# Kernel optimization log

Hardware: AMD Instinct MI355X
Metric: run time of the kernel (lower is better)

The kernel has to match this reference:

```python
import jax, jax.numpy as jnp
import numpy as np

B = 256      # events
N_SV = 64    # secondary vertices per event
N_TRK = 512  # tracks per event
N_PFC = 512  # PF candidates per event
K = 8        # kNN neighbors
H = 32       # hidden dim


def _lin_init(key, fan_in, fan_out):
    k1, k2 = jax.random.split(key)
    lim = 1.0 / np.sqrt(fan_in)
    W = jax.random.uniform(k1, (fan_in, fan_out), minval=-lim, maxval=lim, dtype=jnp.float32)
    b = jax.random.uniform(k2, (fan_out,), minval=-lim, maxval=lim, dtype=jnp.float32)
    return W, b


def setup_inputs() -> dict:
    key = jax.random.key(0)
    ks = jax.random.split(key, 16)
    inp = {
        'x_sv': jax.random.normal(ks[0], (B * N_SV, 14), dtype=jnp.float32),
        'x_trk': jax.random.normal(ks[1], (B * N_TRK, 30), dtype=jnp.float32),
        'x_pfc': jax.random.normal(ks[2], (B * N_PFC, 10), dtype=jnp.float32),
        'batch_sv': jnp.repeat(jnp.arange(B, dtype=jnp.int64), N_SV),
        'batch_trk': jnp.repeat(jnp.arange(B, dtype=jnp.int64), N_TRK),
        'batch_pfc': jnp.repeat(jnp.arange(B, dtype=jnp.int64), N_PFC),
    }
    inp['sv_W1'], inp['sv_b1'] = _lin_init(ks[3], 14, H)
    inp['sv_W2'], inp['sv_b2'] = _lin_init(ks[4], H, H)
    inp['trk_W1'], inp['trk_b1'] = _lin_init(ks[5], 30, H)
    inp['trk_W2'], inp['trk_b2'] = _lin_init(ks[6], H, H)
    inp['pfc_W1'], inp['pfc_b1'] = _lin_init(ks[7], 10, H)
    inp['pfc_W2'], inp['pfc_b2'] = _lin_init(ks[8], H, H)
    inp['conv_W'], inp['conv_b'] = _lin_init(ks[9], 2 * H, H)  # the single shared self.conv
    inp['out_W1'], inp['out_b1'] = _lin_init(ks[10], H, H)
    inp['out_W2'], inp['out_b2'] = _lin_init(ks[11], H, 1)
    return inp


def _encode(x, W1, b1, W2, b2):
    h = jax.nn.elu(x @ W1 + b1)
    return jax.nn.elu(h @ W2 + b2)


def _edge_conv(x_src, x_dst, W, b):
    # x_src [B,Ns,H] source set, x_dst [B,Nd,H] destination/query set.
    # kNN: for each dst node, K nearest src nodes (per event) by Euclidean dist.
    d2 = (jnp.sum(x_dst * x_dst, -1)[:, :, None]
          - 2.0 * jnp.einsum('bnd,bmd->bnm', x_dst, x_src)
          + jnp.sum(x_src * x_src, -1)[:, None, :])  # [B,Nd,Ns]
    _, idx = jax.lax.top_k(-d2, K)                     # [B,Nd,K]
    x_j = jax.vmap(lambda s, i: s[i])(x_src, idx)      # [B,Nd,K,H]
    x_i = jnp.broadcast_to(x_dst[:, :, None, :], x_j.shape)
    e = jnp.concatenate([x_i, x_j - x_i], axis=-1)     # [B,Nd,K,2H]
    m = jax.nn.elu(e @ W + b)                          # edge MLP
    return jnp.max(m, axis=2)                          # max aggregation [B,Nd,H]


def reference(x_sv, x_trk, x_pfc, batch_sv, batch_trk, batch_pfc,
              sv_W1, sv_b1, sv_W2, sv_b2,
              trk_W1, trk_b1, trk_W2, trk_b2,
              pfc_W1, pfc_b1, pfc_W2, pfc_b2,
              conv_W, conv_b, out_W1, out_b1, out_W2, out_b2):
    sv = _encode(x_sv, sv_W1, sv_b1, sv_W2, sv_b2).reshape(B, N_SV, H)
    trk = _encode(x_trk, trk_W1, trk_b1, trk_W2, trk_b2).reshape(B, N_TRK, H)
    pfc = _encode(x_pfc, pfc_W1, pfc_b1, pfc_W2, pfc_b2).reshape(B, N_PFC, H)

    feats1 = _edge_conv(sv, trk, conv_W, conv_b)     # sv -> trk
    feats2 = _edge_conv(pfc, trk, conv_W, conv_b)    # pfc -> trk
    feats3 = _edge_conv(feats1, feats2, conv_W, conv_b)  # feats1 -> feats2 (both trk-sized)

    # avg_pool_x(batch_trk, feats3, batch_trk): per-event mean
    f = feats3.reshape(B * N_TRK, H)
    s = jax.ops.segment_sum(f, batch_trk, num_segments=B)
    cnt = jax.ops.segment_sum(jnp.ones((B * N_TRK,), f.dtype), batch_trk, num_segments=B)
    pooled = s / cnt[:, None]

    out = jax.nn.sigmoid(jax.nn.elu(pooled @ out_W1 + out_b1) @ out_W2 + out_b2)  # [B,1]
    return out, jnp.arange(B, dtype=jnp.int64)
```

## Files before the change

kernel.cpp:

```cpp
#include <hip/hip_runtime.h>
#include <math.h>

#define NB 256
#define KNN 8

typedef __attribute__((ext_vector_type(8))) short short8;
typedef __attribute__((ext_vector_type(4))) float f32x4;

__device__ __forceinline__ float elu_f(float x) {
    return x > 0.f ? x : __expf(x) - 1.f;
}

__device__ __forceinline__ unsigned bf16rn(float x) {
    unsigned u = __float_as_uint(x);
    return (u + 0x7FFFu + ((u >> 16) & 1u)) >> 16;
}

__device__ __forceinline__ void bfsplit(float x, short& h, short& l) {
    unsigned hu = bf16rn(x);
    h = (short)hu;
    l = (short)bf16rn(x - __uint_as_float(hu << 16));
}

__device__ __forceinline__ void cex(unsigned& a, unsigned& b) {
    unsigned lo = min(a, b), hi = max(a, b);
    a = lo; b = hi;
}

__device__ __forceinline__ void sort4(unsigned* s) {
    cex(s[0], s[1]); cex(s[2], s[3]);
    cex(s[0], s[2]); cex(s[1], s[3]);
    cex(s[1], s[2]);
}

__device__ __forceinline__ void merge8_4(unsigned* v, const unsigned* s) {
    v[4] = min(v[4], s[3]); v[5] = min(v[5], s[2]);
    v[6] = min(v[6], s[1]); v[7] = min(v[7], s[0]);
    cex(v[0], v[4]); cex(v[1], v[5]); cex(v[2], v[6]); cex(v[3], v[7]);
    cex(v[0], v[2]); cex(v[1], v[3]); cex(v[4], v[6]); cex(v[5], v[7]);
    cex(v[0], v[1]); cex(v[2], v[3]); cex(v[4], v[5]); cex(v[6], v[7]);
}

__device__ __forceinline__ void merge8(unsigned* v, const unsigned* s) {
#pragma unroll
    for (int i = 0; i < 8; i++) v[i] = min(v[i], s[7 - i]);
    cex(v[0], v[4]); cex(v[1], v[5]); cex(v[2], v[6]); cex(v[3], v[7]);
    cex(v[0], v[2]); cex(v[1], v[3]); cex(v[4], v[6]); cex(v[5], v[7]);
    cex(v[0], v[1]); cex(v[2], v[3]); cex(v[4], v[5]); cex(v[6], v[7]);
}

template<int FIN, int MODE>
__device__ void encode_mfma_body(const float* __restrict__ x,
    const float* __restrict__ W1, const float* __restrict__ b1,
    const float* __restrict__ W2, const float* __restrict__ b2,
    const float* __restrict__ conv_W, const float* __restrict__ conv_b,
    float* __restrict__ enc, float* __restrict__ e1, float* __restrict__ e2,
    unsigned short* __restrict__ hiP, unsigned short* __restrict__ loP,
    float* __restrict__ nrmP,
    int blk, float* __restrict__ sx)
{
    int tid = threadIdx.x;
    int lane = tid & 63, wv = tid >> 6;
    int c = lane & 15, kg = lane >> 4;
    size_t node0 = (size_t)blk * 256;

    {
        const float* xb = x + node0 * FIN;
        for (int i = tid; i < 8192; i += 256) {
            int n = i >> 5, f = i & 31;
            sx[i] = (f < FIN) ? xb[n * FIN + f] : 0.f;
        }
    }
    __syncthreads();

    int rb = wv * 64;

#pragma unroll
    for (int ph = 0; ph < 3; ph++) {
        short8 Bh0, Bl0, Bh1, Bl1;
#pragma unroll
        for (int e = 0; e < 8; e++) {
            int kk = kg * 8 + e;
            float w0, w1;
            if (ph == 0) {
                w0 = (kk < FIN) ? W1[kk * 32 + c] : 0.f;
                w1 = (kk < FIN) ? W1[kk * 32 + 16 + c] : 0.f;
            } else if (ph == 1) {
                w0 = W2[kk * 32 + c];
                w1 = W2[kk * 32 + 16 + c];
            } else {
                w0 = conv_W[1024 + kk * 32 + c];
                w1 = conv_W[1024 + kk * 32 + 16 + c];
                if (MODE == 1) {
                    w0 = conv_W[kk * 32 + c] - w0;
                    w1 = conv_W[kk * 32 + 16 + c] - w1;
                }
            }
            short h, l;
            bfsplit(w0, h, l); Bh0[e] = h; Bl0[e] = l;
            bfsplit(w1, h, l); Bh1[e] = h; Bl1[e] = l;
        }
        float bias0, bias1;
        if (ph == 0)      { bias0 = b1[c]; bias1 = b1[16 + c]; }
        else if (ph == 1) { bias0 = b2[c]; bias1 = b2[16 + c]; }
        else              { bias0 = (MODE == 1) ? conv_b[c] : 0.f;
                            bias1 = (MODE == 1) ? conv_b[16 + c] : 0.f; }

#pragma unroll
        for (int t = 0; t < 4; t++) {
            int tb = rb + t * 16;
            int arow = tb + c;
            const float* ap = sx + arow * 32 + kg * 8;
            float4 a0 = *(const float4*)(ap);
            float4 a1 = *(const float4*)(ap + 4);
            float av[8] = {a0.x, a0.y, a0.z, a0.w, a1.x, a1.y, a1.z, a1.w};
            short8 Ah, Al;
#pragma unroll
            for (int e = 0; e < 8; e++) {
                short h, l;
                bfsplit(av[e], h, l);
                Ah[e] = h; Al[e] = l;
            }

            if (MODE == 0 && ph == 2) {
                float nr = 0.f;
#pragma unroll
                for (int e = 0; e < 8; e++) nr = fmaf(av[e], av[e], nr);
                nr += __shfl_xor(nr, 16);
                nr += __shfl_xor(nr, 32);
                if (kg == 0) nrmP[node0 + arow] = nr;
                *(short8*)(hiP + (node0 + arow) * 32 + kg * 8) = Ah;
                *(short8*)(loP + (node0 + arow) * 32 + kg * 8) = Al;
            }

            f32x4 acc0 = {bias0, bias0, bias0, bias0};
            f32x4 acc1 = {bias1, bias1, bias1, bias1};
            acc0 = __builtin_amdgcn_mfma_f32_16x16x32_bf16(Al, Bh0, acc0, 0, 0, 0);
            acc0 = __builtin_amdgcn_mfma_f32_16x16x32_bf16(Ah, Bl0, acc0, 0, 0, 0);
            acc0 = __builtin_amdgcn_mfma_f32_16x16x32_bf16(Ah, Bh0, acc0, 0, 0, 0);
            acc1 = __builtin_amdgcn_mfma_f32_16x16x32_bf16(Al, Bh1, acc1, 0, 0, 0);
            acc1 = __builtin_amdgcn_mfma_f32_16x16x32_bf16(Ah, Bl1, acc1, 0, 0, 0);
            acc1 = __builtin_amdgcn_mfma_f32_16x16x32_bf16(Ah, Bh1, acc1, 0, 0, 0);

            int drow = tb + kg * 4;
            if (ph < 2) {
#pragma unroll
                for (int r = 0; r < 4; r++) {
                    float v0 = elu_f(acc0[r]);
                    float v1 = elu_f(acc1[r]);
                    sx[(drow + r) * 32 + c] = v0;
                    sx[(drow + r) * 32 + 16 + c] = v1;
                    if (MODE == 1 && ph == 1) {
                        size_t off = (node0 + drow + r) * 32 + c;
                        enc[off] = v0;
                        enc[off + 16] = v1;
                    }
                }
            } else {
#pragma unroll
                for (int r = 0; r < 4; r++) {
                    size_t off = (node0 + drow + r) * 32 + c;
                    e1[off] = acc0[r];
                    e1[off + 16] = acc1[r];
                    if (MODE == 1) {
                        e2[off] = acc0[r];
                        e2[off + 16] = acc1[r];
                    }
                }
            }
        }
    }
}

__global__ __launch_bounds__(256) void encode_all_kernel(
    const float* __restrict__ x_sv, const float* __restrict__ x_trk, const float* __restrict__ x_pfc,
    const float* __restrict__ sv_W1, const float* __restrict__ sv_b1,
    const float* __restrict__ sv_W2, const float* __restrict__ sv_b2,
    const float* __restrict__ trk_W1, const float* __restrict__ trk_b1,
    const float* __restrict__ trk_W2, const float* __restrict__ trk_b2,
    const float* __restrict__ pfc_W1, const float* __restrict__ pfc_b1,
    const float* __restrict__ pfc_W2, const float* __restrict__ pfc_b2,
    const float* __restrict__ conv_W, const float* __restrict__ conv_b,
    float* __restrict__ trk_enc,
    float* __restrict__ Y1, float* __restrict__ Y2,
    float* __restrict__ f1, float* __restrict__ f2,
    unsigned short* __restrict__ svHi, unsigned short* __restrict__ svLo, float* __restrict__ nrm_sv,
    unsigned short* __restrict__ pfcHi, unsigned short* __restrict__ pfcLo, float* __restrict__ nrm_pfc)
{
    __shared__ float sx[8192];
    int bid = blockIdx.x;
    if (bid < 64)
        encode_mfma_body<14, 0>(x_sv, sv_W1, sv_b1, sv_W2, sv_b2, conv_W, conv_b,
                                nullptr, Y1, nullptr, svHi, svLo, nrm_sv, bid, sx);
    else if (bid < 576)
        encode_mfma_body<30, 1>(x_trk, trk_W1, trk_b1, trk_W2, trk_b2, conv_W, conv_b,
                                trk_enc, f1, f2, nullptr, nullptr, nullptr, bid - 64, sx);
    else
        encode_mfma_body<10, 0>(x_pfc, pfc_W1, pfc_b1, pfc_W2, pfc_b2, conv_W, conv_b,
                                nullptr, Y2, nullptr, pfcHi, pfcLo, nrm_pfc, bid - 576, sx);
}

template<int NT>
__device__ void knn_mfma_wave(
    const unsigned short* __restrict__ srcHi, const unsigned short* __restrict__ srcLo,
    const float* __restrict__ snrm,
    const float* __restrict__ dstF,
    int dstbase,
    unsigned short* __restrict__ idx_out)
{
    int lane = threadIdx.x & 63;
    int c = lane & 15, kg = lane >> 4;

    const float* brow = dstF + (size_t)(dstbase + c) * 32 + kg * 8;
    float4 b0 = *(const float4*)(brow);
    float4 b1 = *(const float4*)(brow + 4);
    float bx[8] = {b0.x, b0.y, b0.z, b0.w, b1.x, b1.y, b1.z, b1.w};
    short8 Bh, Bl;
    float nd = 0.f;
#pragma unroll
    for (int i = 0; i < 8; i++) {
        float xv = bx[i];
        nd = fmaf(xv, xv, nd);
        short h, l;
        bfsplit(xv, h, l);
        Bh[i] = h; Bl[i] = l;
    }
    nd += __shfl_xor(nd, 16);
    nd += __shfl_xor(nd, 32);

    unsigned key[8];
#pragma unroll
    for (int k = 0; k < 8; k++) key[k] = 0xFFFFFFFFu;

    for (int t = 0; t < NT; t++) {
        size_t arow = ((size_t)(t * 16 + c)) * 32 + (size_t)kg * 8;
        short8 Ah = *(const short8*)(srcHi + arow);
        short8 Al = *(const short8*)(srcLo + arow);
        f32x4 acc = {0.f, 0.f, 0.f, 0.f};
        acc = __builtin_amdgcn_mfma_f32_16x16x32_bf16(Al, Bl, acc, 0, 0, 0);
        acc = __builtin_amdgcn_mfma_f32_16x16x32_bf16(Al, Bh, acc, 0, 0, 0);
        acc = __builtin_amdgcn_mfma_f32_16x16x32_bf16(Ah, Bl, acc, 0, 0, 0);
        acc = __builtin_amdgcn_mfma_f32_16x16x32_bf16(Ah, Bh, acc, 0, 0, 0);
        float4 sn = *(const float4*)(snrm + t * 16 + kg * 4);
        int sb = t * 16 + kg * 4;
        unsigned cand[4];
        cand[0] = (__float_as_uint(fmaf(-2.f, acc[0], sn.x + nd)) & 0xFFFFFE00u) | (unsigned)(sb + 0);
        cand[1] = (__float_as_uint(fmaf(-2.f, acc[1], sn.y + nd)) & 0xFFFFFE00u) | (unsigned)(sb + 1);
        cand[2] = (__float_as_uint(fmaf(-2.f, acc[2], sn.z + nd)) & 0xFFFFFE00u) | (unsigned)(sb + 2);
        cand[3] = (__float_as_uint(fmaf(-2.f, acc[3], sn.w + nd)) & 0xFFFFFE00u) | (unsigned)(sb + 3);
        sort4(cand); merge8_4(key, cand);
    }

    unsigned oth[8];
#pragma unroll
    for (int k = 0; k < 8; k++) oth[k] = __shfl_xor(key[k], 16);
    merge8(key, oth);
#pragma unroll
    for (int k = 0; k < 8; k++) oth[k] = __shfl_xor(key[k], 32);
    merge8(key, oth);

    if (lane < 16) {
        uint4 o;
        o.x = (key[0] & 511u) | ((key[1] & 511u) << 16);
        o.y = (key[2] & 511u) | ((key[3] & 511u) << 16);
        o.z = (key[4] & 511u) | ((key[5] & 511u) << 16);
        o.w = (key[6] & 511u) | ((key[7] & 511u) << 16);
        *(uint4*)(idx_out + (size_t)(dstbase + c) * 8) = o;
    }
}

__global__ __launch_bounds__(256) void knn12_kernel(
    const unsigned short* __restrict__ svHi, const unsigned short* __restrict__ svLo,
    const float* __restrict__ nrm_sv,
    const unsigned short* __restrict__ pfcHi, const unsigned short* __restrict__ pfcLo,
    const float* __restrict__ nrm_pfc,
    const float* __restrict__ trk_enc,
    unsigned short* __restrict__ idx1, unsigned short* __restrict__ idx2)
{
    int bid = blockIdx.x;
    int wave = threadIdx.x >> 6;
    if (bid < 2048) {
        int e = bid & 255, j = bid >> 8;
        knn_mfma_wave<32>(pfcHi + (size_t)e * 512 * 32, pfcLo + (size_t)e * 512 * 32,
                          nrm_pfc + e * 512, trk_enc + (size_t)e * 512 * 32,
                          j * 64 + wave * 16, idx2 + (size_t)e * 512 * 8);
    } else {
        int b2 = bid - 2048;
        int e = b2 & 255, j = b2 >> 8;
        knn_mfma_wave<4>(svHi + (size_t)e * 64 * 32, svLo + (size_t)e * 64 * 32,
                         nrm_sv + e * 64, trk_enc + (size_t)e * 512 * 32,
                         j * 64 + wave * 16, idx1 + (size_t)e * 512 * 8);
    }
}

__global__ __launch_bounds__(256) void knn3_kernel(
    const unsigned short* __restrict__ f1Hi, const unsigned short* __restrict__ f1Lo,
    const float* __restrict__ nrm_f1,
    const float* __restrict__ f2,
    unsigned short* __restrict__ idx3)
{
    int bid = blockIdx.x;
    int wave = threadIdx.x >> 6;
    int e = bid & 255, j = bid >> 8;
    knn_mfma_wave<32>(f1Hi + (size_t)e * 512 * 32, f1Lo + (size_t)e * 512 * 32,
                      nrm_f1 + e * 512, f2 + (size_t)e * 512 * 32,
                      j * 64 + wave * 16, idx3 + (size_t)e * 512 * 8);
}

__device__ __forceinline__ void maxgather(const float* __restrict__ Ybase,
                                          const int* rows, float4* m)
{
    const float4* Yb = (const float4*)Ybase;
    const float4* r0 = Yb + (size_t)rows[0] * 8;
#pragma unroll
    for (int q = 0; q < 8; q++) m[q] = r0[q];
#pragma unroll
    for (int k = 1; k < 8; k++) {
        const float4* rr = Yb + (size_t)rows[k] * 8;
#pragma unroll
        for (int q = 0; q < 8; q++) {
            float4 v = rr[q];
            m[q].x = fmaxf(m[q].x, v.x); m[q].y = fmaxf(m[q].y, v.y);
            m[q].z = fmaxf(m[q].z, v.z); m[q].w = fmaxf(m[q].w, v.w);
        }
    }
}

__device__ __forceinline__ void decode_rows(const unsigned short* __restrict__ ip,
                                            size_t t, int* rows)
{
    uint4 u = *(const uint4*)(ip + t * 8);
    rows[0] = (int)(u.x & 0xffff); rows[1] = (int)(u.x >> 16);
    rows[2] = (int)(u.y & 0xffff); rows[3] = (int)(u.y >> 16);
    rows[4] = (int)(u.z & 0xffff); rows[5] = (int)(u.z >> 16);
    rows[6] = (int)(u.w & 0xffff); rows[7] = (int)(u.w >> 16);
}

__global__ __launch_bounds__(256) void g12_kernel(
    const float* __restrict__ Y1, const unsigned short* __restrict__ idx1, float* __restrict__ f1,
    const float* __restrict__ Y2, const unsigned short* __restrict__ idx2, float* __restrict__ f2,
    unsigned short* __restrict__ f1Hi, unsigned short* __restrict__ f1Lo,
    float* __restrict__ nrm_f1)
{
    int bid = blockIdx.x;
    int tid = threadIdx.x;
    int rows[8];
    float* fp;
    const float* Yb;
    int t;
    int isf1 = (bid < 512);
    if (isf1) {
        t = bid * 256 + tid;
        decode_rows(idx1, (size_t)t, rows);
        Yb = Y1 + (size_t)(t >> 9) * 64 * 32;
        fp = f1 + (size_t)t * 32;
    } else {
        t = (bid - 512) * 256 + tid;
        decode_rows(idx2, (size_t)t, rows);
        Yb = Y2 + (size_t)(t >> 9) * 512 * 32;
        fp = f2 + (size_t)t * 32;
    }
    float4 m[8];
    maxgather(Yb, rows, m);
    float4* op = (float4*)fp;
    float4 r[8];
#pragma unroll
    for (int q = 0; q < 8; q++) {
        float4 bv = op[q];
        r[q].x = elu_f(bv.x + m[q].x); r[q].y = elu_f(bv.y + m[q].y);
        r[q].z = elu_f(bv.z + m[q].z); r[q].w = elu_f(bv.w + m[q].w);
        op[q] = r[q];
    }
    if (isf1) {
        unsigned hw[16], lw[16];
        float nr = 0.f;
#pragma unroll
        for (int q = 0; q < 8; q++) {
            float4 v = r[q];
            nr = fmaf(v.x, v.x, nr); nr = fmaf(v.y, v.y, nr);
            nr = fmaf(v.z, v.z, nr); nr = fmaf(v.w, v.w, nr);
            unsigned h0 = bf16rn(v.x), h1 = bf16rn(v.y), h2 = bf16rn(v.z), h3 = bf16rn(v.w);
            unsigned l0 = bf16rn(v.x - __uint_as_float(h0 << 16));
            unsigned l1 = bf16rn(v.y - __uint_as_float(h1 << 16));
            unsigned l2 = bf16rn(v.z - __uint_as_float(h2 << 16));
            unsigned l3 = bf16rn(v.w - __uint_as_float(h3 << 16));
            hw[2*q]   = h0 | (h1 << 16); hw[2*q+1] = h2 | (h3 << 16);
            lw[2*q]   = l0 | (l1 << 16); lw[2*q+1] = l2 | (l3 << 16);
        }
        nrm_f1[t] = nr;
        uint4* hp = (uint4*)(f1Hi + (size_t)t * 32);
        uint4* lp = (uint4*)(f1Lo + (size_t)t * 32);
#pragma unroll
        for (int q = 0; q < 4; q++) {
            hp[q] = make_uint4(hw[4*q], hw[4*q+1], hw[4*q+2], hw[4*q+3]);
            lp[q] = make_uint4(lw[4*q], lw[4*q+1], lw[4*q+2], lw[4*q+3]);
        }
    }
}

__global__ __launch_bounds__(256) void yb3_kernel(
    const float* __restrict__ f1, const float* __restrict__ f2,
    const float* __restrict__ conv_W, const float* __restrict__ conv_b,
    float* __restrict__ Y3, float* __restrict__ B3)
{
    __shared__ float sx[8][32];
    int bid = blockIdx.x;
    int tid = threadIdx.x;
    int mode = (bid >= 2048);
    const float* X = mode ? f2 : f1;
    float* O = mode ? B3 : Y3;
    int rb = (mode ? bid - 2048 : bid) * 64;
    int ln = tid >> 5, c = tid & 31;
    float wcol[32];
#pragma unroll
    for (int d = 0; d < 32; d++)
        wcol[d] = mode ? (conv_W[d * 32 + c] - conv_W[1024 + d * 32 + c])
                       : conv_W[1024 + d * 32 + c];
    float bias = mode ? conv_b[c] : 0.f;
    for (int p = 0; p < 8; p++) {
        __syncthreads();
        sx[ln][c] = X[(size_t)(rb + p * 8 + ln) * 32 + c];
        __syncthreads();
        const float4* hr = (const float4*)(&sx[ln][0]);
        float acc = bias;
#pragma unroll
        for (int q = 0; q < 8; q++) {
            float4 hh = hr[q];
            acc = fmaf(hh.x, wcol[q * 4 + 0], acc);
            acc = fmaf(hh.y, wcol[q * 4 + 1], acc);
            acc = fmaf(hh.z, wcol[q * 4 + 2], acc);
            acc = fmaf(hh.w, wcol[q * 4 + 3], acc);
        }
        O[(size_t)(rb + p * 8 + ln) * 32 + c] = acc;
    }
}

__global__ __launch_bounds__(256) void g3_kernel(
    const float* __restrict__ Y3, const float* __restrict__ B3,
    const unsigned short* __restrict__ idx3,
    float* __restrict__ pool)
{
    __shared__ float sp[4][32];
    int bid = blockIdx.x;
    int tid = threadIdx.x, lane = tid & 63, wave = tid >> 6;
    int t = bid * 256 + tid;
    int e = t >> 9;
    int rows[8];
    decode_rows(idx3, (size_t)t, rows);
    float4 m[8];
    maxgather(Y3 + (size_t)e * 512 * 32, rows, m);
    const float4* bp = (const float4*)(B3 + (size_t)t * 32);
    float4 r[8];
#pragma unroll
    for (int q = 0; q < 8; q++) {
        float4 bv = bp[q];
        r[q].x = elu_f(bv.x + m[q].x); r[q].y = elu_f(bv.y + m[q].y);
        r[q].z = elu_f(bv.z + m[q].z); r[q].w = elu_f(bv.w + m[q].w);
    }
    for (int off = 1; off < 64; off <<= 1) {
#pragma unroll
        for (int q = 0; q < 8; q++) {
            r[q].x += __shfl_xor(r[q].x, off);
            r[q].y += __shfl_xor(r[q].y, off);
            r[q].z += __shfl_xor(r[q].z, off);
            r[q].w += __shfl_xor(r[q].w, off);
        }
    }
    if (lane == 0) {
#pragma unroll
        for (int q = 0; q < 8; q++) {
            sp[wave][q*4+0] = r[q].x; sp[wave][q*4+1] = r[q].y;
            sp[wave][q*4+2] = r[q].z; sp[wave][q*4+3] = r[q].w;
        }
    }
    __syncthreads();
    if (tid < 32)
        pool[(size_t)bid * 32 + tid] = sp[0][tid] + sp[1][tid] + sp[2][tid] + sp[3][tid];
}

__global__ __launch_bounds__(64) void final_kernel(
    const float* __restrict__ pool,
    const float* __restrict__ W1, const float* __restrict__ b1,
    const float* __restrict__ W2, const float* __restrict__ b2,
    float* __restrict__ outp)
{
    int b = blockIdx.x;
    int lane = threadIdx.x, c = lane & 31;
    __shared__ float sp[32];
    __shared__ float sh1[32];
    if (lane < 32)
        sp[c] = (pool[(size_t)(2*b) * 32 + c] + pool[(size_t)(2*b+1) * 32 + c]) * (1.0f / 512.0f);
    __syncthreads();
    if (lane < 32) {
        float h = b1[c];
#pragma unroll
        for (int d = 0; d < 32; d++) h = fmaf(sp[d], W1[d * 32 + c], h);
        sh1[c] = elu_f(h);
    }
    __syncthreads();
    if (lane == 0) {
        float o = b2[0];
#pragma unroll
        for (int d = 0; d < 32; d++) o = fmaf(sh1[d], W2[d], o);
        o = 1.f / (1.f + __expf(-o));
        outp[b] = o;
        outp[NB + b] = (float)b;
    }
}

extern "C" void kernel_launch(void* const* d_in, const int* in_sizes, int n_in,
                              void* d_out, int out_size, void* d_ws, size_t ws_size,
                              hipStream_t stream) {
    const float* x_sv  = (const float*)d_in[0];
    const float* x_trk = (const float*)d_in[1];
    const float* x_pfc = (const float*)d_in[2];
    const float* sv_W1  = (const float*)d_in[6];
    const float* sv_b1  = (const float*)d_in[7];
    const float* sv_W2  = (const float*)d_in[8];
    const float* sv_b2  = (const float*)d_in[9];
    const float* trk_W1 = (const float*)d_in[10];
    const float* trk_b1 = (const float*)d_in[11];
    const float* trk_W2 = (const float*)d_in[12];
    const float* trk_b2 = (const float*)d_in[13];
    const float* pfc_W1 = (const float*)d_in[14];
    const float* pfc_b1 = (const float*)d_in[15];
    const float* pfc_W2 = (const float*)d_in[16];
    const float* pfc_b2 = (const float*)d_in[17];
    const float* conv_W = (const float*)d_in[18];
    const float* conv_b = (const float*)d_in[19];
    const float* out_W1 = (const float*)d_in[20];
    const float* out_b1 = (const float*)d_in[21];
    const float* out_W2 = (const float*)d_in[22];
    const float* out_b2 = (const float*)d_in[23];

    float* ws = (float*)d_ws;
    const size_t SV_E  = (size_t)NB * 64 * 32;
    const size_t TRK_E = (size_t)NB * 512 * 32;
    float* f1      = ws;
    float* f2      = f1 + TRK_E;
    float* trk_enc = f2 + TRK_E;
    float* Y1      = trk_enc + TRK_E;
    float* Y2      = Y1 + SV_E;
    unsigned short* svHi  = (unsigned short*)(Y2 + TRK_E);
    unsigned short* svLo  = svHi + SV_E;
    unsigned short* pfcHi = svLo + SV_E;
    unsigned short* pfcLo = pfcHi + TRK_E;
    unsigned short* f1Hi  = pfcLo + TRK_E;
    unsigned short* f1Lo  = f1Hi + TRK_E;
    float* nrm_sv  = (float*)(f1Lo + TRK_E);
    float* nrm_pfc = nrm_sv + (size_t)NB * 64;
    float* nrm_f1  = nrm_pfc + (size_t)NB * 512;
    unsigned short* idx1 = (unsigned short*)(nrm_f1 + (size_t)NB * 512);
    unsigned short* idx2 = idx1 + (size_t)NB * 512 * 8;
    unsigned short* idx3 = idx2 + (size_t)NB * 512 * 8;
    float* Y3   = trk_enc;
    float* B3   = (float*)pfcHi;
    float* pool = (float*)svHi;

    encode_all_kernel<<<1088, 256, 0, stream>>>(
        x_sv, x_trk, x_pfc,
        sv_W1, sv_b1, sv_W2, sv_b2,
        trk_W1, trk_b1, trk_W2, trk_b2,
        pfc_W1, pfc_b1, pfc_W2, pfc_b2,
        conv_W, conv_b,
        trk_enc, Y1, Y2, f1, f2,
        svHi, svLo, nrm_sv, pfcHi, pfcLo, nrm_pfc);

    knn12_kernel<<<4096, 256, 0, stream>>>(svHi, svLo, nrm_sv,
                                           pfcHi, pfcLo, nrm_pfc,
                                           trk_enc, idx1, idx2);
    g12_kernel<<<1024, 256, 0, stream>>>(Y1, idx1, f1, Y2, idx2, f2,
                                         f1Hi, f1Lo, nrm_f1);

    yb3_kernel<<<4096, 256, 0, stream>>>(f1, f2, conv_W, conv_b, Y3, B3);
    knn3_kernel<<<2048, 256, 0, stream>>>(f1Hi, f1Lo, nrm_f1, f2, idx3);
    g3_kernel<<<512, 256, 0, stream>>>(Y3, B3, idx3, pool);

    final_kernel<<<NB, 64, 0, stream>>>(pool, out_W1, out_b1, out_W2, out_b2, (float*)d_out);
}
```

Baseline: 337.3 us.

## Merge kNN candidate batches, fuse sv/pfc kNN per block, MFMA yb3 projection

```diff
diff --git a/kernel.cpp b/kernel.cpp
--- a/kernel.cpp
+++ b/kernel.cpp
@@ -27,18 +27,13 @@
     a = lo; b = hi;
 }
 
-__device__ __forceinline__ void sort4(unsigned* s) {
-    cex(s[0], s[1]); cex(s[2], s[3]);
-    cex(s[0], s[2]); cex(s[1], s[3]);
-    cex(s[1], s[2]);
-}
-
-__device__ __forceinline__ void merge8_4(unsigned* v, const unsigned* s) {
-    v[4] = min(v[4], s[3]); v[5] = min(v[5], s[2]);
-    v[6] = min(v[6], s[1]); v[7] = min(v[7], s[0]);
-    cex(v[0], v[4]); cex(v[1], v[5]); cex(v[2], v[6]); cex(v[3], v[7]);
-    cex(v[0], v[2]); cex(v[1], v[3]); cex(v[4], v[6]); cex(v[5], v[7]);
-    cex(v[0], v[1]); cex(v[2], v[3]); cex(v[4], v[5]); cex(v[6], v[7]);
+__device__ __forceinline__ void sort8(unsigned* s) {
+    cex(s[0], s[1]); cex(s[2], s[3]); cex(s[4], s[5]); cex(s[6], s[7]);
+    cex(s[0], s[2]); cex(s[1], s[3]); cex(s[4], s[6]); cex(s[5], s[7]);
+    cex(s[1], s[2]); cex(s[5], s[6]);
+    cex(s[0], s[4]); cex(s[1], s[5]); cex(s[2], s[6]); cex(s[3], s[7]);
+    cex(s[2], s[4]); cex(s[3], s[5]);
+    cex(s[1], s[2]); cex(s[3], s[4]); cex(s[5], s[6]);
 }
 
 __device__ __forceinline__ void merge8(unsigned* v, const unsigned* s) {
@@ -200,23 +195,15 @@
                                 nullptr, Y2, nullptr, pfcHi, pfcLo, nrm_pfc, bid - 576, sx);
 }
 
-template<int NT>
-__device__ void knn_mfma_wave(
-    const unsigned short* __restrict__ srcHi, const unsigned short* __restrict__ srcLo,
-    const float* __restrict__ snrm,
-    const float* __restrict__ dstF,
-    int dstbase,
-    unsigned short* __restrict__ idx_out)
-{
-    int lane = threadIdx.x & 63;
-    int c = lane & 15, kg = lane >> 4;
-
+__device__ __forceinline__ void knn_build_B(const float* __restrict__ dstF,
+                                            int dstbase, int c, int kg,
+                                            short8& Bh, short8& Bl, float& nd)
+{
     const float* brow = dstF + (size_t)(dstbase + c) * 32 + kg * 8;
     float4 b0 = *(const float4*)(brow);
     float4 b1 = *(const float4*)(brow + 4);
     float bx[8] = {b0.x, b0.y, b0.z, b0.w, b1.x, b1.y, b1.z, b1.w};
-    short8 Bh, Bl;
-    float nd = 0.f;
+    nd = 0.f;
 #pragma unroll
     for (int i = 0; i < 8; i++) {
         float xv = bx[i];
@@ -227,30 +214,44 @@
     }
     nd += __shfl_xor(nd, 16);
     nd += __shfl_xor(nd, 32);
-
-    unsigned key[8];
-#pragma unroll
-    for (int k = 0; k < 8; k++) key[k] = 0xFFFFFFFFu;
-
-    for (int t = 0; t < NT; t++) {
-        size_t arow = ((size_t)(t * 16 + c)) * 32 + (size_t)kg * 8;
-        short8 Ah = *(const short8*)(srcHi + arow);
-        short8 Al = *(const short8*)(srcLo + arow);
-        f32x4 acc = {0.f, 0.f, 0.f, 0.f};
-        acc = __builtin_amdgcn_mfma_f32_16x16x32_bf16(Al, Bl, acc, 0, 0, 0);
-        acc = __builtin_amdgcn_mfma_f32_16x16x32_bf16(Al, Bh, acc, 0, 0, 0);
-        acc = __builtin_amdgcn_mfma_f32_16x16x32_bf16(Ah, Bl, acc, 0, 0, 0);
-        acc = __builtin_amdgcn_mfma_f32_16x16x32_bf16(Ah, Bh, acc, 0, 0, 0);
-        float4 sn = *(const float4*)(snrm + t * 16 + kg * 4);
-        int sb = t * 16 + kg * 4;
-        unsigned cand[4];
-        cand[0] = (__float_as_uint(fmaf(-2.f, acc[0], sn.x + nd)) & 0xFFFFFE00u) | (unsigned)(sb + 0);
-        cand[1] = (__float_as_uint(fmaf(-2.f, acc[1], sn.y + nd)) & 0xFFFFFE00u) | (unsigned)(sb + 1);
-        cand[2] = (__float_as_uint(fmaf(-2.f, acc[2], sn.z + nd)) & 0xFFFFFE00u) | (unsigned)(sb + 2);
-        cand[3] = (__float_as_uint(fmaf(-2.f, acc[3], sn.w + nd)) & 0xFFFFFE00u) | (unsigned)(sb + 3);
-        sort4(cand); merge8_4(key, cand);
-    }
-
+}
+
+template<int NT>
+__device__ __forceinline__ void knn_scan(
+    const unsigned short* __restrict__ srcHi, const unsigned short* __restrict__ srcLo,
+    const float* __restrict__ snrm,
+    short8 Bh, short8 Bl, float nd, int c, int kg,
+    unsigned* key)
+{
+    for (int t = 0; t < NT; t += 2) {
+        unsigned cand[8];
+#pragma unroll
+        for (int u = 0; u < 2; u++) {
+            int tt = t + u;
+            size_t arow = ((size_t)(tt * 16 + c)) * 32 + (size_t)kg * 8;
+            short8 Ah = *(const short8*)(srcHi + arow);
+            short8 Al = *(const short8*)(srcLo + arow);
+            f32x4 acc = {0.f, 0.f, 0.f, 0.f};
+            acc = __builtin_amdgcn_mfma_f32_16x16x32_bf16(Al, Bl, acc, 0, 0, 0);
+            acc = __builtin_amdgcn_mfma_f32_16x16x32_bf16(Al, Bh, acc, 0, 0, 0);
+            acc = __builtin_amdgcn_mfma_f32_16x16x32_bf16(Ah, Bl, acc, 0, 0, 0);
+            acc = __builtin_amdgcn_mfma_f32_16x16x32_bf16(Ah, Bh, acc, 0, 0, 0);
+            float4 sn = *(const float4*)(snrm + tt * 16 + kg * 4);
+            int sb = tt * 16 + kg * 4;
+            cand[u*4+0] = (__float_as_uint(fmaf(-2.f, acc[0], sn.x + nd)) & 0xFFFFFE00u) | (unsigned)(sb + 0);
+            cand[u*4+1] = (__float_as_uint(fmaf(-2.f, acc[1], sn.y + nd)) & 0xFFFFFE00u) | (unsigned)(sb + 1);
+            cand[u*4+2] = (__float_as_uint(fmaf(-2.f, acc[2], sn.z + nd)) & 0xFFFFFE00u) | (unsigned)(sb + 2);
+            cand[u*4+3] = (__float_as_uint(fmaf(-2.f, acc[3], sn.w + nd)) & 0xFFFFFE00u) | (unsigned)(sb + 3);
+        }
+        sort8(cand);
+        merge8(key, cand);
+    }
+}
+
+__device__ __forceinline__ void knn_finalize(unsigned* key, int lane,
+                                             unsigned short* __restrict__ idx_out,
+                                             int dstbase)
+{
     unsigned oth[8];
 #pragma unroll
     for (int k = 0; k < 8; k++) oth[k] = __shfl_xor(key[k], 16);
@@ -258,14 +259,13 @@
 #pragma unroll
     for (int k = 0; k < 8; k++) oth[k] = __shfl_xor(key[k], 32);
     merge8(key, oth);
-
     if (lane < 16) {
         uint4 o;
         o.x = (key[0] & 511u) | ((key[1] & 511u) << 16);
         o.y = (key[2] & 511u) | ((key[3] & 511u) << 16);
         o.z = (key[4] & 511u) | ((key[5] & 511u) << 16);
         o.w = (key[6] & 511u) | ((key[7] & 511u) << 16);
-        *(uint4*)(idx_out + (size_t)(dstbase + c) * 8) = o;
+        *(uint4*)(idx_out + (size_t)(dstbase + lane) * 8) = o;
     }
 }
 
@@ -278,19 +278,27 @@
     unsigned short* __restrict__ idx1, unsigned short* __restrict__ idx2)
 {
     int bid = blockIdx.x;
-    int wave = threadIdx.x >> 6;
-    if (bid < 2048) {
-        int e = bid & 255, j = bid >> 8;
-        knn_mfma_wave<32>(pfcHi + (size_t)e * 512 * 32, pfcLo + (size_t)e * 512 * 32,
-                          nrm_pfc + e * 512, trk_enc + (size_t)e * 512 * 32,
-                          j * 64 + wave * 16, idx2 + (size_t)e * 512 * 8);
-    } else {
-        int b2 = bid - 2048;
-        int e = b2 & 255, j = b2 >> 8;
-        knn_mfma_wave<4>(svHi + (size_t)e * 64 * 32, svLo + (size_t)e * 64 * 32,
-                         nrm_sv + e * 64, trk_enc + (size_t)e * 512 * 32,
-                         j * 64 + wave * 16, idx1 + (size_t)e * 512 * 8);
-    }
+    int e = bid & 255, j = bid >> 8;
+    int lane = threadIdx.x & 63, wave = threadIdx.x >> 6;
+    int c = lane & 15, kg = lane >> 4;
+    int dstbase = j * 64 + wave * 16;
+
+    short8 Bh, Bl;
+    float nd;
+    knn_build_B(trk_enc + (size_t)e * 512 * 32, dstbase, c, kg, Bh, Bl, nd);
+
+    unsigned key[8];
+#pragma unroll
+    for (int k = 0; k < 8; k++) key[k] = 0xFFFFFFFFu;
+    knn_scan<32>(pfcHi + (size_t)e * 512 * 32, pfcLo + (size_t)e * 512 * 32,
+                 nrm_pfc + e * 512, Bh, Bl, nd, c, kg, key);
+    knn_finalize(key, lane, idx2 + (size_t)e * 512 * 8, dstbase);
+
+#pragma unroll
+    for (int k = 0; k < 8; k++) key[k] = 0xFFFFFFFFu;
+    knn_scan<4>(svHi + (size_t)e * 64 * 32, svLo + (size_t)e * 64 * 32,
+                nrm_sv + e * 64, Bh, Bl, nd, c, kg, key);
+    knn_finalize(key, lane, idx1 + (size_t)e * 512 * 8, dstbase);
 }
 
 __global__ __launch_bounds__(256) void knn3_kernel(
@@ -300,11 +308,21 @@
     unsigned short* __restrict__ idx3)
 {
     int bid = blockIdx.x;
-    int wave = threadIdx.x >> 6;
     int e = bid & 255, j = bid >> 8;
-    knn_mfma_wave<32>(f1Hi + (size_t)e * 512 * 32, f1Lo + (size_t)e * 512 * 32,
-                      nrm_f1 + e * 512, f2 + (size_t)e * 512 * 32,
-                      j * 64 + wave * 16, idx3 + (size_t)e * 512 * 8);
+    int lane = threadIdx.x & 63, wave = threadIdx.x >> 6;
+    int c = lane & 15, kg = lane >> 4;
+    int dstbase = j * 64 + wave * 16;
+
+    short8 Bh, Bl;
+    float nd;
+    knn_build_B(f2 + (size_t)e * 512 * 32, dstbase, c, kg, Bh, Bl, nd);
+
+    unsigned key[8];
+#pragma unroll
+    for (int k = 0; k < 8; k++) key[k] = 0xFFFFFFFFu;
+    knn_scan<32>(f1Hi + (size_t)e * 512 * 32, f1Lo + (size_t)e * 512 * 32,
+                 nrm_f1 + e * 512, Bh, Bl, nd, c, kg, key);
+    knn_finalize(key, lane, idx3 + (size_t)e * 512 * 8, dstbase);
 }
 
 __device__ __forceinline__ void maxgather(const float* __restrict__ Ybase,
@@ -403,35 +421,63 @@
     const float* __restrict__ conv_W, const float* __restrict__ conv_b,
     float* __restrict__ Y3, float* __restrict__ B3)
 {
-    __shared__ float sx[8][32];
     int bid = blockIdx.x;
-    int tid = threadIdx.x;
-    int mode = (bid >= 2048);
+    int mode = (bid >= 512);
     const float* X = mode ? f2 : f1;
     float* O = mode ? B3 : Y3;
-    int rb = (mode ? bid - 2048 : bid) * 64;
-    int ln = tid >> 5, c = tid & 31;
-    float wcol[32];
-#pragma unroll
-    for (int d = 0; d < 32; d++)
-        wcol[d] = mode ? (conv_W[d * 32 + c] - conv_W[1024 + d * 32 + c])
-                       : conv_W[1024 + d * 32 + c];
-    float bias = mode ? conv_b[c] : 0.f;
-    for (int p = 0; p < 8; p++) {
-        __syncthreads();
-        sx[ln][c] = X[(size_t)(rb + p * 8 + ln) * 32 + c];
-        __syncthreads();
-        const float4* hr = (const float4*)(&sx[ln][0]);
-        float acc = bias;
-#pragma unroll
-        for (int q = 0; q < 8; q++) {
-            float4 hh = hr[q];
-            acc = fmaf(hh.x, wcol[q * 4 + 0], acc);
-            acc = fmaf(hh.y, wcol[q * 4 + 1], acc);
-            acc = fmaf(hh.z, wcol[q * 4 + 2], acc);
-            acc = fmaf(hh.w, wcol[q * 4 + 3], acc);
-        }
-        O[(size_t)(rb + p * 8 + ln) * 32 + c] = acc;
+    size_t node0 = (size_t)(mode ? bid - 512 : bid) * 256;
+    int tid = threadIdx.x, lane = tid & 63, wv = tid >> 6;
+    int c = lane & 15, kg = lane >> 4;
+
+    short8 Bh0, Bl0, Bh1, Bl1;
+#pragma unroll
+    for (int e = 0; e < 8; e++) {
+        int kk = kg * 8 + e;
+        float w0 = conv_W[1024 + kk * 32 + c];
+        float w1 = conv_W[1024 + kk * 32 + 16 + c];
+        if (mode) {
+            w0 = conv_W[kk * 32 + c] - w0;
+            w1 = conv_W[kk * 32 + 16 + c] - w1;
+        }
+        short h, l;
+        bfsplit(w0, h, l); Bh0[e] = h; Bl0[e] = l;
+        bfsplit(w1, h, l); Bh1[e] = h; Bl1[e] = l;
+    }
+    float bias0 = mode ? conv_b[c] : 0.f;
+    float bias1 = mode ? conv_b[16 + c] : 0.f;
+
+    int rb = wv * 64;
+#pragma unroll
+    for (int t = 0; t < 4; t++) {
+        int tb = rb + t * 16;
+        int arow = tb + c;
+        const float* ap = X + (node0 + arow) * 32 + kg * 8;
+        float4 a0 = *(const float4*)(ap);
+        float4 a1 = *(const float4*)(ap + 4);
+        float av[8] = {a0.x, a0.y, a0.z, a0.w, a1.x, a1.y, a1.z, a1.w};
+        short8 Ah, Al;
+#pragma unroll
+        for (int e = 0; e < 8; e++) {
+            short h, l;
+            bfsplit(av[e], h, l);
+            Ah[e] = h; Al[e] = l;
+        }
+        f32x4 acc0 = {bias0, bias0, bias0, bias0};
+        f32x4 acc1 = {bias1, bias1, bias1, bias1};
+        acc0 = __builtin_amdgcn_mfma_f32_16x16x32_bf16(Al, Bh0, acc0, 0, 0, 0);
+        acc0 = __builtin_amdgcn_mfma_f32_16x16x32_bf16(Ah, Bl0, acc0, 0, 0, 0);
+        acc0 = __builtin_amdgcn_mfma_f32_16x16x32_bf16(Ah, Bh0, acc0, 0, 0, 0);
+        acc1 = __builtin_amdgcn_mfma_f32_16x16x32_bf16(Al, Bh1, acc1, 0, 0, 0);
+        acc1 = __builtin_amdgcn_mfma_f32_16x16x32_bf16(Ah, Bl1, acc1, 0, 0, 0);
+        acc1 = __builtin_amdgcn_mfma_f32_16x16x32_bf16(Ah, Bh1, acc1, 0, 0, 0);
+
+        int drow = tb + kg * 4;
+#pragma unroll
+        for (int r = 0; r < 4; r++) {
+            size_t off = (node0 + drow + r) * 32 + c;
+            O[off] = acc0[r];
+            O[off + 16] = acc1[r];
+        }
     }
 }
 
@@ -566,13 +612,13 @@
         trk_enc, Y1, Y2, f1, f2,
         svHi, svLo, nrm_sv, pfcHi, pfcLo, nrm_pfc);
 
-    knn12_kernel<<<4096, 256, 0, stream>>>(svHi, svLo, nrm_sv,
+    knn12_kernel<<<2048, 256, 0, stream>>>(svHi, svLo, nrm_sv,
                                            pfcHi, pfcLo, nrm_pfc,
                                            trk_enc, idx1, idx2);
     g12_kernel<<<1024, 256, 0, stream>>>(Y1, idx1, f1, Y2, idx2, f2,
                                          f1Hi, f1Lo, nrm_f1);
 
-    yb3_kernel<<<4096, 256, 0, stream>>>(f1, f2, conv_W, conv_b, Y3, B3);
+    yb3_kernel<<<1024, 256, 0, stream>>>(f1, f2, conv_W, conv_b, Y3, B3);
     knn3_kernel<<<2048, 256, 0, stream>>>(f1Hi, f1Lo, nrm_f1, f2, idx3);
     g3_kernel<<<512, 256, 0, stream>>>(Y3, B3, idx3, pool);
 
```

Result: faster. 316.3 us (-6.2%).
